# Kernel optimization log

Measured on AMD Instinct MI355X. Metric: run time of the kernel, lower is better.

The kernel has to match this reference:

```python
import jax, jax.numpy as jnp
import numpy as np

N_HEAD = 8


def setup_inputs() -> dict:
    key = jax.random.key(0)
    ks = jax.random.split(key, 12)
    b, l, d_q, d_o, h, w = 32, 64, 1024, 512, 32, 32

    def rn(k, shape, s=0.02):
        return jax.random.normal(k, shape, jnp.float32) * s

    return {
        "q": jax.random.normal(ks[0], (b, l, d_q), jnp.float32),
        "v": jax.random.normal(ks[1], (b, d_o, h, w), jnp.float32),
        "mask": jax.random.bernoulli(ks[2], 0.2, (b, l)),
        "w_qs_w": rn(ks[3], (d_o, d_q)), "w_qs_b": jnp.zeros((d_o,), jnp.float32),
        "w_qs_att_w": rn(ks[4], (1, d_o)), "w_qs_att_b": jnp.zeros((1,), jnp.float32),
        "w_kc_w": rn(ks[5], (d_o, d_o, 1, 1)), "w_kc_b": jnp.zeros((d_o,), jnp.float32),
        "w_kd_w": rn(ks[6], (d_o, d_o, 1, 1)), "w_kd_b": jnp.zeros((d_o,), jnp.float32),
        "w_vs_w": rn(ks[7], (d_o, d_o, 1, 1)), "w_vs_b": jnp.zeros((d_o,), jnp.float32),
        "w_m_w": rn(ks[8], (1, d_o, 3, 3)), "w_m_b": jnp.zeros((1,), jnp.float32),
        "bn_gamma": jnp.ones((d_o,), jnp.float32), "bn_beta": jnp.zeros((d_o,), jnp.float32),
        "bn_mean": jnp.zeros((d_o,), jnp.float32), "bn_var": jnp.ones((d_o,), jnp.float32),
    }


def _conv1x1(x, wgt, bias):  # x: (b,c,h,w), wgt: (o,c,1,1)
    return jnp.einsum('bchw,oc->bohw', x, wgt[:, :, 0, 0]) + bias[None, :, None, None]


def reference(q, v, mask, w_qs_w, w_qs_b, w_qs_att_w, w_qs_att_b,
              w_kc_w, w_kc_b, w_kd_w, w_kd_b, w_vs_w, w_vs_b,
              w_m_w, w_m_b, bn_gamma, bn_beta, bn_mean, bn_var):
    b, l, _ = q.shape
    _, c, h, w_ = v.shape
    n = N_HEAD
    dk = c // n
    temp = float(np.power(dk, 0.5))  # sqrt(d_o // n_head)
    residual = v

    qp = q @ w_qs_w.T + w_qs_b                       # (b,l,d_o)
    flap = qp @ w_qs_att_w.T + w_qs_att_b            # (b,l,1)
    flap = jnp.where(mask[:, :, None], -1e9, flap)
    flap = jax.nn.softmax(flap, axis=-1)             # softmax over size-1 dim -> all ones (faithful to torch)

    kc = _conv1x1(v, w_kc_w, w_kc_b).reshape(b, n, dk, h * w_).transpose(0, 1, 3, 2)  # (b,n,hw,dk)
    kd = _conv1x1(v, w_kd_w, w_kd_b).reshape(b, n, dk, h * w_).transpose(0, 1, 3, 2)
    vh = _conv1x1(v, w_vs_w, w_vs_b).reshape(b, n, dk, h * w_).transpose(0, 1, 3, 2)
    qh = qp.reshape(b, l, n, dk).transpose(0, 2, 1, 3)                                 # (b,n,l,dk)

    # Collect: bmm -> weight by flap -> reduce over l -> softmax over hw -> bmm with v
    attn_col = jnp.einsum('bnld,bnsd->bnls', qh, kc)                 # (b,n,l,hw)
    attn_col = (attn_col * flap[:, None, :, :]).sum(axis=2, keepdims=True) / temp  # (b,n,1,hw)
    attn_col = jax.nn.softmax(attn_col, axis=-1)
    attn = jnp.einsum('bnus,bnsd->bnud', attn_col, vh)               # (b,n,1,dk)

    # Diffuse: bmm -> weight by flap^T -> reduce over l -> sigmoid -> outer product
    attn_dif = jnp.einsum('bnsd,bnld->bnsl', kd, qh)                 # (b,n,hw,l)
    flap_t = flap.transpose(0, 2, 1)[:, None]                        # (b,1,1,l)
    attn_dif = jax.nn.sigmoid((attn_dif * flap_t).sum(-1, keepdims=True) / temp)  # (b,n,hw,1)
    output = attn_dif * attn                                         # (b,n,hw,dk)

    # Faithful to torch permute(0,1,4,3,2).view(b,-1,h,w) (requires h==w)
    out = output.reshape(b, n, h, w_, dk).transpose(0, 1, 4, 3, 2).reshape(b, c, h, w_)
    attn_map = out

    m = jax.lax.conv_general_dilated(out, w_m_w, (1, 1), 'SAME',
                                     dimension_numbers=('NCHW', 'OIHW', 'NCHW'))
    m_attn = (m + w_m_b[None, :, None, None]).reshape(b, h * w_)

    eps = 1e-5  # BatchNorm2d eval mode
    scale = bn_gamma / jnp.sqrt(bn_var + eps)
    out = (out - bn_mean[None, :, None, None]) * scale[None, :, None, None] + bn_beta[None, :, None, None]
    out = out + residual
    out = jnp.where(out >= 0, out, 0.1 * out)  # LeakyReLU(0.1)
    return (out, m_attn, attn_map)
```

## Files before the change

kernel.cpp:

```cpp
#include <hip/hip_runtime.h>


#define BB 32
#define LL 64
#define DQn 1024
#define CCn 512
#define NH 8
#define DKn 64
#define HWn 1024
#define NBLK 512
#define SLOTSTRIDE 16

typedef unsigned short u16;
typedef unsigned int u32;
typedef unsigned long long u64;

__device__ __forceinline__ float bfr(u16 u) {
    return __uint_as_float(((u32)u) << 16);
}
__device__ __forceinline__ u16 f2bf(float f) {
    u32 x = __float_as_uint(f);
    u32 r = (x + 0x7FFFu + ((x >> 16) & 1u)) >> 16;
    return (u16)r;
}

__device__ __forceinline__ void cst(float* p, float v) {
    __hip_atomic_store(p, v, __ATOMIC_RELAXED, __HIP_MEMORY_SCOPE_AGENT);
}
__device__ __forceinline__ u32 cldu(const u32* p) {
    return __hip_atomic_load(const_cast<u32*>(p), __ATOMIC_RELAXED,
                             __HIP_MEMORY_SCOPE_AGENT);
}
__device__ __forceinline__ void cstu(u32* p, u32 v) {
    __hip_atomic_store(p, v, __ATOMIC_RELAXED, __HIP_MEMORY_SCOPE_AGENT);
}

#define POOLB 78080

struct MArgs {
    const float *q, *v, *wqs, *bqs, *wkc, *bkc, *wkd, *bkd, *wvs, *bvs, *wm, *wmb,
                *gam, *bet, *mea, *var;
    float *qsp, *qs, *wq, *bq, *dsig, *sums, *attn, *A2g, *pvp;
    u32* bar;
    float *out0, *out1, *out2;
};

__device__ __forceinline__ void gbar(u32* bar, int i) {
    u32* slots = bar + 16;
    u32 epoch = (u32)(i + 1);
    __syncthreads();
    int t = threadIdx.x;
    if (blockIdx.x == (u32)(NBLK - 1)) {
        if (t < 64) {
            if (t == 0) cstu(&slots[(NBLK - 1) * SLOTSTRIDE], epoch);
            int base = t * (NBLK / 64);
            int it = 0;
            for (;;) {
                bool ok = true;
#pragma unroll
                for (int k = 0; k < NBLK / 64; ++k)
                    ok = ok && (cldu(&slots[(base + k) * SLOTSTRIDE]) == epoch);
                if (__all(ok)) break;
                __builtin_amdgcn_s_sleep(1);
                if (++it > (1 << 15)) break;
            }
            if (t == 0) cstu(&bar[8 + i], 1u);
        }
    } else if (t == 0) {
        cstu(&slots[blockIdx.x * SLOTSTRIDE], epoch);
        int it = 0;
        while (cldu(&bar[8 + i]) == 0u) {
            __builtin_amdgcn_s_sleep(2);
            if (++it > (1 << 18)) break;
        }
    }
    __syncthreads();
    __builtin_amdgcn_fence(__ATOMIC_ACQUIRE, "agent");
}

__global__ void kinit(u32* bar) {
    int t = threadIdx.x + blockIdx.x * blockDim.x;
    int total = 16 + NBLK * SLOTSTRIDE;
    for (int i = t; i < total; i += blockDim.x * gridDim.x)
        cstu(&bar[i], 0u);
}

#define PVACC(accv, eA, eB, vf) \
    accv[0] += eA.x * (vf); accv[1] += eA.y * (vf); accv[2] += eA.z * (vf); accv[3] += eA.w * (vf); \
    accv[4] += eB.x * (vf); accv[5] += eB.y * (vf); accv[6] += eB.z * (vf); accv[7] += eB.w * (vf);

__global__ void __launch_bounds__(256, 2) mega(MArgs A) {
    extern __shared__ char pool[];
    u32*   vtd = (u32*)pool;
    float* red = (float*)(pool + 65536);
    float* etb = (float*)(pool + 69888);
    float* ext = (float*)(pool + 71936);
    float* scr2  = red;
    float* pvl   = etb;
    float* scr7  = red;
    float* al7   = red + 320;
    float* sinvp = red + 384;
    float* dsl   = red;
    float* A2l   = red + 512;
    u16*   k8s   = (u16*)etb;
    float* al    = ext;
    float* bnA   = ext + 512;
    float* bnB   = ext + 1024;

    int t = threadIdx.x;
    int bid = blockIdx.x;
    int sc = bid & 15, b = bid >> 4;
    int s0 = sc * 64;

    if (bid < 128) {
        int b1 = bid >> 2;
        int dq = (bid & 3) * 256 + t;
        const float* qp = A.q + (size_t)b1 * LL * DQn + dq;
        float acc = 0.f;
#pragma unroll 8
        for (int l = 0; l < LL; ++l) acc += qp[l * DQn];
        cst(&A.qsp[b1 * DQn + dq], acc);
    }

    {
        int sp = t & 31, c2 = t >> 5;
        const float* vb = A.v + (((size_t)(b * CCn + c2 * 64)) << 10) + s0 + sp * 2;
#pragma unroll 8
        for (int cr = 0; cr < 64; ++cr) {
            int r = c2 * 64 + cr;
            float2 xv = *reinterpret_cast<const float2*>(vb + ((size_t)cr << 10));
            u32 w = (u32)f2bf(xv.x) | ((u32)f2bf(xv.y) << 16);
            vtd[r * 32 + (sp ^ (r & 31))] = w;
        }
    }
    gbar(A.bar, 0);

    {
        int dof = bid;
        int b2 = t & 31, ch = t >> 5;
        const float* wrow = A.wqs + (size_t)dof * DQn + ch * 128;
        const float* qrow = A.qsp + (size_t)b2 * DQn + ch * 128;
        float acc = 0.f;
#pragma unroll 8
        for (int i = 0; i < 128; i += 4) {
            float4 wv = *reinterpret_cast<const float4*>(wrow + i);
            float4 qv = *reinterpret_cast<const float4*>(qrow + i);
            acc += wv.x * qv.x + wv.y * qv.y + wv.z * qv.z + wv.w * qv.w;
        }
        scr2[t] = acc;
        __syncthreads();
        if (t < 32) {
            float a = 0.f;
#pragma unroll
            for (int c2 = 0; c2 < 8; ++c2) a += scr2[c2 * 32 + t];
            cst(&A.qs[t * CCn + dof], a + 64.f * A.bqs[dof]);
        }
    }
    gbar(A.bar, 1);

    {
        float2 p = *reinterpret_cast<const float2*>(&A.qs[b * CCn + t * 2]);
        etb[t * 2] = p.x; etb[t * 2 + 1] = p.y;
    }
    __syncthreads();

    if (sc == 0 && t < 16) {
        int wsel = t >> 3, n = t & 7;
        const float* bw = wsel ? A.bkd : A.bkc;
        float a2 = 0.f;
#pragma unroll 8
        for (int d = 0; d < DKn; ++d)
            a2 += etb[n * DKn + d] * bw[n * DKn + d];
        cst(&A.bq[wsel * 256 + b * 8 + n], a2);
    }

    {
        int cl = t & 31, n3 = t >> 5;
        int c = sc * 32 + cl;
#pragma unroll
        for (int wsel = 0; wsel < 2; ++wsel) {
            const float* w = wsel ? A.wkd : A.wkc;
            const float* qrow = etb + n3 * DKn;
            const float* wrow = w + (size_t)(n3 * DKn) * CCn + c;
            float acc = 0.f;
#pragma unroll 8
            for (int d = 0; d < DKn; ++d) acc += qrow[d] * wrow[(size_t)d * CCn];
            cst(&A.wq[((size_t)b * CCn + c) * 16 + wsel * 8 + n3], acc);
        }
    }
    for (int i = t; i < 64 * 17; i += 256) red[i] = 0.f;
    gbar(A.bar, 2);

    {
        float* wqL = etb;
        int s = t & 63, g2 = t >> 6;
        int sp = s >> 1, sh = (s & 1) << 4;
        float ak[16];
#pragma unroll
        for (int j = 0; j < 16; ++j) ak[j] = 0.f;
#pragma unroll 1
        for (int cc4 = 0; cc4 < 4; ++cc4) {
            __syncthreads();
            {
                const float* src = A.wq + (((size_t)b * CCn + cc4 * 128) << 4) + t * 8;
                float4 p0 = *reinterpret_cast<const float4*>(src);
                float4 p1 = *reinterpret_cast<const float4*>(src + 4);
                float* dst = wqL + t * 8;
                dst[0] = p0.x; dst[1] = p0.y; dst[2] = p0.z; dst[3] = p0.w;
                dst[4] = p1.x; dst[5] = p1.y; dst[6] = p1.z; dst[7] = p1.w;
            }
            __syncthreads();
#pragma unroll 4
            for (int i = 0; i < 32; ++i) {
                int cl = g2 * 32 + i;
                int r = cc4 * 128 + cl;
                u32 wv = vtd[r * 32 + (sp ^ (r & 31))];
                float vvf = bfr((u16)(wv >> sh));
                const float* wc = wqL + cl * 16;
#pragma unroll
                for (int j = 0; j < 16; ++j) ak[j] += wc[j] * vvf;
            }
        }
#pragma unroll
        for (int j = 0; j < 16; ++j) atomicAdd(&red[s * 17 + j], ak[j]);
    }
    __syncthreads();
    if (t < 64) {
        int s = t;
#pragma unroll
        for (int n = 0; n < NH; ++n) {
            float rc = red[s * 17 + n];
            float rd = red[s * 17 + 8 + n];
            float skc = (rc + A.bq[b * 8 + n]) * 0.125f;
            float skd = (rd + A.bq[256 + b * 8 + n]) * 0.125f;
            etb[s * 8 + n] = __expf(skc);
            cst(&A.dsig[((size_t)(b * NH + n)) * HWn + s0 + s],
                1.f / (1.f + __expf(-skd)));
        }
    }
    __syncthreads();
    if (t < 8) {
        float a = 0.f;
#pragma unroll
        for (int s = 0; s < 64; ++s) a += etb[s * 8 + t];
        cst(&A.sums[(b * NH + t) * 16 + sc], a);
    }
    {
        float acc0[NH], acc1[NH];
#pragma unroll
        for (int n = 0; n < NH; ++n) { acc0[n] = 0.f; acc1[n] = 0.f; }
        int c0 = t, c1 = t + 256;
        int m = t & 31;
#pragma unroll 2
        for (int sp = 0; sp < 32; ++sp) {
            u32 w0 = vtd[c0 * 32 + (sp ^ m)];
            u32 w1 = vtd[c1 * 32 + (sp ^ m)];
            float va0 = bfr((u16)(w0 & 0xffffu)), va1 = bfr((u16)(w0 >> 16));
            float vb0 = bfr((u16)(w1 & 0xffffu)), vb1 = bfr((u16)(w1 >> 16));
            float4 e0a = *reinterpret_cast<const float4*>(etb + sp * 16);
            float4 e0b = *reinterpret_cast<const float4*>(etb + sp * 16 + 4);
            float4 e1a = *reinterpret_cast<const float4*>(etb + sp * 16 + 8);
            float4 e1b = *reinterpret_cast<const float4*>(etb + sp * 16 + 12);
            PVACC(acc0, e0a, e0b, va0)
            PVACC(acc0, e1a, e1b, va1)
            PVACC(acc1, e0a, e0b, vb0)
            PVACC(acc1, e1a, e1b, vb1)
        }
        size_t base = ((size_t)sc * BB + b) * NH;
#pragma unroll
        for (int n = 0; n < NH; ++n) {
            cst(&A.pvp[(base + n) * CCn + c0], acc0[n]);
            cst(&A.pvp[(base + n) * CCn + c1], acc1[n]);
        }
    }
    gbar(A.bar, 3);

    if (bid < 256) {
        int n = bid & 7, b7 = bid >> 3;
        for (int c = t; c < CCn; c += 256) {
            float acc = 0.f;
#pragma unroll 4
            for (int s2 = 0; s2 < 16; ++s2)
                acc += A.pvp[(((size_t)s2 * BB + b7) * NH + n) * CCn + c];
            pvl[c] = acc;
        }
        if (t == 0) {
            float a = 0.f;
#pragma unroll
            for (int s2 = 0; s2 < 16; ++s2)
                a += A.sums[(b7 * NH + n) * 16 + s2];
            sinvp[0] = 1.f / a;
        }
        __syncthreads();
        {
            int d = t & 63, qq = t >> 6;
            const float* wrow = A.wvs + (size_t)(n * DKn + d) * CCn + qq * 128;
            const float* pq = pvl + qq * 128;
            float acc = 0.f;
#pragma unroll 4
            for (int i = 0; i < 128; ++i) acc += pq[i] * wrow[i];
            scr7[d * 5 + qq] = acc;
        }
        __syncthreads();
        if (t < 64) {
            float a = (scr7[t * 5] + scr7[t * 5 + 1] + scr7[t * 5 + 2] + scr7[t * 5 + 3])
                      * sinvp[0] + A.bvs[n * DKn + t];
            cst(&A.attn[(b7 * NH + n) * DKn + t], a);
            al7[t] = a;
        }
        __syncthreads();
        if (t < 9) {
            float acc = 0.f;
#pragma unroll 8
            for (int d2 = 0; d2 < DKn; ++d2)
                acc += al7[d2] * A.wm[(n * DKn + d2) * 9 + t];
            cst(&A.A2g[b7 * 72 + n * 9 + t], acc);
        }
    }
    gbar(A.bar, 4);

    int y0 = sc * 2;
    {
        for (int idx = t; idx < CCn; idx += 256) {
            al[idx] = A.attn[b * CCn + idx];
            float Av = A.gam[idx] * rsqrtf(A.var[idx] + 1e-5f);
            bnA[idx] = Av;
            bnB[idx] = A.bet[idx] - A.mea[idx] * Av;
        }
        for (int idx = t; idx < NH * 64; idx += 256) {
            int n = idx >> 6, r6 = idx & 63;
            int yb2 = r6 >> 5, x = r6 & 31;
            dsl[idx] = A.dsig[((size_t)(b * NH + n)) * HWn + x * 32 + y0 + yb2];
        }
        for (int idx = t; idx < 4 * NH * 32; idx += 256) {
            int ry = idx >> 8, n = (idx >> 5) & 7, x = idx & 31;
            int ycol = y0 - 1 + ry;
            float dvv = 0.f;
            if ((unsigned)ycol < 32u)
                dvv = A.dsig[((size_t)(b * NH + n)) * HWn + x * 32 + ycol];
            k8s[idx] = f2bf(dvv);
        }
        if (t < 72) A2l[t] = A.A2g[b * 72 + t];
    }
    __syncthreads();
    {
        int l = t & 63, wv = t >> 6;
        int csub = l >> 4, yb = (l >> 3) & 1, x0 = (l & 7) * 4;
        int sl = yb * 32 + x0;
#pragma unroll 2
        for (int it = 0; it < 32; ++it) {
            int c = it * 16 + wv * 4 + csub;
            int n = c >> 6;
            int m = c & 31;
            u32 w0 = vtd[c * 32 + ((sl >> 1) ^ m)];
            u32 w1 = vtd[c * 32 + (((sl >> 1) + 1) ^ m)];
            float4 dv = *reinterpret_cast<const float4*>(dsl + n * 64 + sl);
            float a = al[c], Ac = bnA[c], Bc = bnB[c];
            float p0 = a * dv.x, p1 = a * dv.y, p2 = a * dv.z, p3 = a * dv.w;
            size_t ob = (((size_t)(b * CCn + c)) << 10) + (u32)((y0 + yb) * 32 + x0);
            *reinterpret_cast<float4*>(A.out2 + ob) = make_float4(p0, p1, p2, p3);
            float o0 = fmaf(p0, Ac, Bc) + bfr((u16)(w0 & 0xffffu));
            float o1 = fmaf(p1, Ac, Bc) + bfr((u16)(w0 >> 16));
            float o2 = fmaf(p2, Ac, Bc) + bfr((u16)(w1 & 0xffffu));
            float o3 = fmaf(p3, Ac, Bc) + bfr((u16)(w1 >> 16));
            o0 = o0 < 0.f ? 0.1f * o0 : o0;
            o1 = o1 < 0.f ? 0.1f * o1 : o1;
            o2 = o2 < 0.f ? 0.1f * o2 : o2;
            o3 = o3 < 0.f ? 0.1f * o3 : o3;
            *reinterpret_cast<float4*>(A.out0 + ob) = make_float4(o0, o1, o2, o3);
        }
    }
    if (t < 64) {
        int y = y0 + (t >> 5), x = t & 31;
        float msum = 0.f;
#pragma unroll
        for (int n = 0; n < NH; ++n) {
#pragma unroll
            for (int dy = 0; dy < 3; ++dy) {
                int ry = (t >> 5) + dy;
#pragma unroll
                for (int dx = 0; dx < 3; ++dx) {
                    int xx = x + dx - 1;
                    if ((unsigned)xx < 32u)
                        msum += A2l[n * 9 + dy * 3 + dx] * bfr(k8s[ry * 256 + n * 32 + xx]);
                }
            }
        }
        A.out1[b * HWn + y * 32 + x] = msum + A.wmb[0];
    }
}


__global__ void k1_qsum_pre(const float* __restrict__ q, float* __restrict__ qsp) {
    int b = blockIdx.y;
    int dq = blockIdx.x * 256 + threadIdx.x;
    const float* qp = q + (size_t)b * LL * DQn + dq;
    float acc = 0.f;
#pragma unroll 8
    for (int l = 0; l < LL; ++l) acc += qp[l * DQn];
    qsp[b * DQn + dq] = acc;
}

__global__ void k2_qsum(const float* __restrict__ qsp, const float* __restrict__ w,
                        const float* __restrict__ bias, float* __restrict__ qs) {
    int dof = blockIdx.x;
    int t = threadIdx.x;
    int b = t & 31, ch = t >> 5;
    const float* wrow = w + (size_t)dof * DQn + ch * 128;
    const float* qrow = qsp + (size_t)b * DQn + ch * 128;
    float acc = 0.f;
#pragma unroll 8
    for (int i = 0; i < 128; i += 4) {
        float4 wv = *reinterpret_cast<const float4*>(wrow + i);
        float4 qv = *reinterpret_cast<const float4*>(qrow + i);
        acc += wv.x * qv.x + wv.y * qv.y + wv.z * qv.z + wv.w * qv.w;
    }
    __shared__ float scr[256];
    scr[t] = acc;
    __syncthreads();
    if (t < 32) {
        float a = 0.f;
#pragma unroll
        for (int c2 = 0; c2 < 8; ++c2) a += scr[c2 * 32 + t];
        qs[t * CCn + dof] = a + 64.f * bias[dof];
    }
}

__global__ void k3_wq(const float* __restrict__ qs,
                      const float* __restrict__ wkc, const float* __restrict__ bkc,
                      const float* __restrict__ wkd, const float* __restrict__ bkd,
                      float* __restrict__ wq, float* __restrict__ bq) {
    int cc = blockIdx.x, wsel = blockIdx.y, b = blockIdx.z;
    const float* w = wsel ? wkd : wkc;
    int cl = threadIdx.x & 31, n = threadIdx.x >> 5;
    int c = cc * 32 + cl;
    const float* qrow = qs + b * CCn + n * DKn;
    const float* wrow = w + (size_t)(n * DKn) * CCn + c;
    float acc = 0.f;
#pragma unroll 8
    for (int d = 0; d < DKn; ++d)
        acc += qrow[d] * wrow[(size_t)d * CCn];
    wq[((size_t)b * CCn + c) * 16 + wsel * 8 + n] = acc;
    if (cc == 0 && b == 0) {
        const float* bw = wsel ? bkd : bkc;
        int pp = threadIdx.x, bb = pp >> 3, nn = pp & 7;
        float a2 = 0.f;
#pragma unroll 8
        for (int d = 0; d < DKn; ++d)
            a2 += qs[bb * CCn + nn * DKn + d] * bw[nn * DKn + d];
        bq[wsel * 256 + pp] = a2;
    }
}

__global__ void __launch_bounds__(256) k46_scorepv(
        const float* __restrict__ v, const float* __restrict__ wq,
        const float* __restrict__ bq, float* __restrict__ dsig,
        float* __restrict__ pvp, float* __restrict__ sums) {
    int sc = blockIdx.x, b = blockIdx.y;
    __shared__ u16 vt[CCn * 33];
    __shared__ float red[4][32][17];
    __shared__ float et[32 * 8];
    int t = threadIdx.x;
    int s0 = sc * 32;
    {
        int s = t & 31, c2 = t >> 5;
        const float* vb = v + ((size_t)(b * CCn + c2 * 64) << 10) + s0 + s;
#pragma unroll 8
        for (int cr = 0; cr < 64; ++cr)
            vt[(c2 * 64 + cr) * 33 + s] = f2bf(vb[(size_t)cr << 10]);
    }
    __syncthreads();
    {
        int s = t & 31, g = t >> 5;
        float ak[16];
#pragma unroll
        for (int j = 0; j < 16; ++j) ak[j] = 0.f;
        const float* wqb = wq + ((size_t)b * CCn + g * 64) * 16;
#pragma unroll 4
        for (int i = 0; i < 64; ++i) {
            float vv = bfr(vt[(g * 64 + i) * 33 + s]);
            const float* wc = wqb + i * 16;
#pragma unroll
            for (int j = 0; j < 16; ++j) ak[j] += wc[j] * vv;
        }
#pragma unroll
        for (int j = 0; j < 16; ++j) ak[j] += __shfl_xor(ak[j], 32);
        int wv = t >> 6;
        if ((t & 63) < 32) {
#pragma unroll
            for (int j = 0; j < 16; ++j) red[wv][s][j] = ak[j];
        }
    }
    __syncthreads();
    if (t < 32) {
        int s = t;
#pragma unroll
        for (int n = 0; n < NH; ++n) {
            float rc = red[0][s][n] + red[1][s][n] + red[2][s][n] + red[3][s][n];
            float rd = red[0][s][8 + n] + red[1][s][8 + n] + red[2][s][8 + n] + red[3][s][8 + n];
            float skc = (rc + bq[b * 8 + n]) * 0.125f;
            float skd = (rd + bq[256 + b * 8 + n]) * 0.125f;
            et[s * 8 + n] = __expf(skc);
            dsig[(b * NH + n) * HWn + s0 + s] = 1.f / (1.f + __expf(-skd));
        }
    }
    __syncthreads();
    if (t < 8) {
        float a = 0.f;
#pragma unroll
        for (int s = 0; s < 32; ++s) a += et[s * 8 + t];
        sums[(b * NH + t) * 32 + sc] = a;
    }
    {
        float acc0[NH], acc1[NH];
#pragma unroll
        for (int n = 0; n < NH; ++n) { acc0[n] = 0.f; acc1[n] = 0.f; }
#pragma unroll 2
        for (int s = 0; s < 32; ++s) {
            float4 ea = *reinterpret_cast<const float4*>(et + s * 8);
            float4 eb = *reinterpret_cast<const float4*>(et + s * 8 + 4);
            float va = bfr(vt[t * 33 + s]);
            float vb2 = bfr(vt[(t + 256) * 33 + s]);
            acc0[0] += ea.x * va; acc0[1] += ea.y * va; acc0[2] += ea.z * va; acc0[3] += ea.w * va;
            acc0[4] += eb.x * va; acc0[5] += eb.y * va; acc0[6] += eb.z * va; acc0[7] += eb.w * va;
            acc1[0] += ea.x * vb2; acc1[1] += ea.y * vb2; acc1[2] += ea.z * vb2; acc1[3] += ea.w * vb2;
            acc1[4] += eb.x * vb2; acc1[5] += eb.y * vb2; acc1[6] += eb.z * vb2; acc1[7] += eb.w * vb2;
        }
        size_t base = ((size_t)sc * BB + b) * NH;
#pragma unroll
        for (int n = 0; n < NH; ++n) {
            pvp[(base + n) * CCn + t] = acc0[n];
            pvp[(base + n) * CCn + t + 256] = acc1[n];
        }
    }
}

__global__ void k7_attn(const float* __restrict__ pvp, const float* __restrict__ sums,
                        const float* __restrict__ wvs, const float* __restrict__ bvs,
                        float* __restrict__ attn) {
    int n = blockIdx.x, b = blockIdx.y;
    __shared__ float pvl[CCn];
    __shared__ float scr[64 * 5];
    __shared__ float sinv;
    int t = threadIdx.x;
    if (t == 0) {
        float a = 0.f;
#pragma unroll
        for (int sc = 0; sc < 32; ++sc) a += sums[(b * NH + n) * 32 + sc];
        sinv = 1.f / a;
    }
    for (int c = t; c < CCn; c += 256) {
        float acc = 0.f;
#pragma unroll 4
        for (int sc = 0; sc < 32; ++sc)
            acc += pvp[(((size_t)sc * BB + b) * NH + n) * CCn + c];
        pvl[c] = acc;
    }
    __syncthreads();
    int d = t & 63, qq = t >> 6;
    const float* wrow = wvs + (size_t)(n * DKn + d) * CCn + qq * 128;
    const float* pq = pvl + qq * 128;
    float acc = 0.f;
#pragma unroll 4
    for (int i = 0; i < 128; ++i) acc += pq[i] * wrow[i];
    scr[d * 5 + qq] = acc;
    __syncthreads();
    if (t < 64) {
        float a = (scr[t * 5] + scr[t * 5 + 1] + scr[t * 5 + 2] + scr[t * 5 + 3]) * sinv
                + bvs[n * DKn + t];
        attn[(b * NH + n) * DKn + t] = a;
    }
}

__global__ void k8_mattn(const float* __restrict__ dsig, const float* __restrict__ attn,
                         const float* __restrict__ wm, const float* __restrict__ wmb,
                         float* __restrict__ out1) {
    int b = blockIdx.x;
    __shared__ float dst[NH * 1056];
    __shared__ float al[CCn];
    __shared__ float A2[NH * 9];
    int t = threadIdx.x;
    al[t] = attn[b * CCn + t];
    al[t + 256] = attn[b * CCn + t + 256];
    for (int g = t; g < NH * HWn; g += 256) {
        int n = g >> 10, s = g & 1023;
        dst[n * 1056 + (s & 31) * 33 + (s >> 5)] = dsig[b * NH * HWn + g];
    }
    __syncthreads();
    if (t < 72) {
        int n = t / 9, tap = t % 9;
        float acc = 0.f;
#pragma unroll 8
        for (int d = 0; d < DKn; ++d)
            acc += al[n * DKn + d] * wm[(n * DKn + d) * 9 + tap];
        A2[t] = acc;
    }
    __syncthreads();
    float bm = wmb[0];
    for (int pos = t; pos < HWn; pos += 256) {
        int y = pos >> 5, x = pos & 31;
        float m = 0.f;
#pragma unroll
        for (int n = 0; n < NH; ++n) {
            const float* dn = dst + n * 1056;
#pragma unroll
            for (int dy = 0; dy < 3; ++dy) {
                int yy = y + dy - 1;
                if ((unsigned)yy < 32u) {
#pragma unroll
                    for (int dx = 0; dx < 3; ++dx) {
                        int xx = x + dx - 1;
                        if ((unsigned)xx < 32u)
                            m += A2[n * 9 + dy * 3 + dx] * dn[yy * 33 + xx];
                    }
                }
            }
        }
        out1[b * HWn + pos] = m + bm;
    }
}

__global__ void __launch_bounds__(256) k9_out(
        const float* __restrict__ v, const float* __restrict__ dsig,
        const float* __restrict__ attn,
        const float* __restrict__ gamma, const float* __restrict__ beta,
        const float* __restrict__ mean, const float* __restrict__ var,
        float* __restrict__ out0, float* __restrict__ out2) {
    int dh = blockIdx.x, n = blockIdx.y, b = blockIdx.z;
    __shared__ float dst[1056];
    __shared__ float al[16], bnA[16], bnB[16];
    int t = threadIdx.x;
#pragma unroll
    for (int k = 0; k < 4; ++k) {
        int s = t + k * 256;
        dst[(s & 31) * 33 + (s >> 5)] = dsig[(b * NH + n) * HWn + s];
    }
    if (t < 16) {
        int d = dh * 16 + t;
        al[t] = attn[(b * NH + n) * DKn + d];
        int ch = n * DKn + d;
        float A = gamma[ch] * rsqrtf(var[ch] + 1e-5f);
        bnA[t] = A;
        bnB[t] = beta[ch] - mean[ch] * A;
    }
    __syncthreads();
    int y = t >> 3, x = (t & 7) * 4;
    const float* dr = dst + y * 33 + x;
#pragma unroll 2
    for (int k = 0; k < 16; ++k) {
        int d = dh * 16 + k;
        size_t base = (((size_t)(b * CCn + n * DKn + d)) << 10) + y * 32 + x;
        float4 v4 = *reinterpret_cast<const float4*>(v + base);
        float a = al[k], A = bnA[k], Bc = bnB[k];
        float p0 = a * dr[0], p1 = a * dr[1], p2 = a * dr[2], p3 = a * dr[3];
        float4 mo = make_float4(p0, p1, p2, p3);
        *reinterpret_cast<float4*>(out2 + base) = mo;
        float o0 = p0 * A + Bc + v4.x;
        float o1 = p1 * A + Bc + v4.y;
        float o2 = p2 * A + Bc + v4.z;
        float o3 = p3 * A + Bc + v4.w;
        o0 = o0 < 0.f ? 0.1f * o0 : o0;
        o1 = o1 < 0.f ? 0.1f * o1 : o1;
        o2 = o2 < 0.f ? 0.1f * o2 : o2;
        o3 = o3 < 0.f ? 0.1f * o3 : o3;
        float4 oo = make_float4(o0, o1, o2, o3);
        *reinterpret_cast<float4*>(out0 + base) = oo;
    }
}

extern "C" void kernel_launch(void* const* d_in, const int* in_sizes, int n_in,
                              void* d_out, int out_size, void* d_ws, size_t ws_size,
                              hipStream_t stream) {
    (void)in_sizes; (void)n_in; (void)out_size; (void)ws_size;
    const float* q   = (const float*)d_in[0];
    const float* v   = (const float*)d_in[1];
    const float* wqs = (const float*)d_in[3];
    const float* bqs = (const float*)d_in[4];
    const float* wkc = (const float*)d_in[7];
    const float* bkc = (const float*)d_in[8];
    const float* wkd = (const float*)d_in[9];
    const float* bkd = (const float*)d_in[10];
    const float* wvs = (const float*)d_in[11];
    const float* bvs = (const float*)d_in[12];
    const float* wm  = (const float*)d_in[13];
    const float* wmb = (const float*)d_in[14];
    const float* gam = (const float*)d_in[15];
    const float* bet = (const float*)d_in[16];
    const float* mea = (const float*)d_in[17];
    const float* var = (const float*)d_in[18];

    float* ws = (float*)d_ws;
    float* out0 = (float*)d_out;
    float* out1 = out0 + 16777216;
    float* out2 = out1 + 32768;

    static int mode = -1;
    if (mode < 0) {
        hipError_t e = hipFuncSetAttribute(reinterpret_cast<const void*>(mega),
                                           hipFuncAttributeMaxDynamicSharedMemorySize,
                                           POOLB);
        mode = (e == hipSuccess) ? 1 : 0;
    }

    if (mode == 1) {
        MArgs a;
        a.q = q; a.v = v; a.wqs = wqs; a.bqs = bqs; a.wkc = wkc; a.bkc = bkc;
        a.wkd = wkd; a.bkd = bkd; a.wvs = wvs; a.bvs = bvs; a.wm = wm; a.wmb = wmb;
        a.gam = gam; a.bet = bet; a.mea = mea; a.var = var;
        a.qsp  = ws;
        a.qs   = ws + 32768;
        a.wq   = ws + 49152;
        a.bq   = ws + 311296;
        a.dsig = ws + 311808;
        a.sums = ws + 573952;
        a.attn = ws + 578048;
        a.A2g  = ws + 594432;
        a.pvp  = ws + 596736;
        a.bar  = (u32*)(ws + 2693888);
        a.out0 = out0; a.out1 = out1; a.out2 = out2;
        kinit<<<dim3(8), dim3(256), 0, stream>>>(a.bar);
        mega<<<dim3(NBLK), dim3(256), POOLB, stream>>>(a);
        return;
    }

    float* qsp  = ws + 0;
    float* qs   = ws + 32768;
    float* wq   = ws + 49152;
    float* bq   = ws + 311296;
    float* dsig = ws + 311808;
    float* sums = ws + 573952;
    float* attn = ws + 582144;
    float* pvp  = ws + 598528;

    k1_qsum_pre<<<dim3(4, 32), 256, 0, stream>>>(q, qsp);
    k2_qsum<<<dim3(512), 256, 0, stream>>>(qsp, wqs, bqs, qs);
    k3_wq<<<dim3(16, 2, 32), 256, 0, stream>>>(qs, wkc, bkc, wkd, bkd, wq, bq);
    k46_scorepv<<<dim3(32, 32), 256, 0, stream>>>(v, wq, bq, dsig, pvp, sums);
    k7_attn<<<dim3(8, 32), 256, 0, stream>>>(pvp, sums, wvs, bvs, attn);
    k8_mattn<<<dim3(32), 256, 0, stream>>>(dsig, attn, wm, wmb, out1);
    k9_out<<<dim3(4, 8, 32), 256, 0, stream>>>(v, dsig, attn, gam, bet, mea, var, out0, out2);
}
```

Before: 401.6 us.

## Replace grid-wide barriers with per-batch 16-block group barriers

```diff
diff --git a/kernel.cpp b/kernel.cpp
--- a/kernel.cpp
+++ b/kernel.cpp
@@ -45,42 +45,28 @@
     float *out0, *out1, *out2;
 };
 
-__device__ __forceinline__ void gbar(u32* bar, int i) {
-    u32* slots = bar + 16;
+__device__ __forceinline__ void gbarb(u32* slots, int b, int sc, int i) {
     u32 epoch = (u32)(i + 1);
     __syncthreads();
     int t = threadIdx.x;
-    if (blockIdx.x == (u32)(NBLK - 1)) {
-        if (t < 64) {
-            if (t == 0) cstu(&slots[(NBLK - 1) * SLOTSTRIDE], epoch);
-            int base = t * (NBLK / 64);
-            int it = 0;
-            for (;;) {
-                bool ok = true;
-#pragma unroll
-                for (int k = 0; k < NBLK / 64; ++k)
-                    ok = ok && (cldu(&slots[(base + k) * SLOTSTRIDE]) == epoch);
-                if (__all(ok)) break;
-                __builtin_amdgcn_s_sleep(1);
-                if (++it > (1 << 15)) break;
-            }
-            if (t == 0) cstu(&bar[8 + i], 1u);
-        }
-    } else if (t == 0) {
-        cstu(&slots[blockIdx.x * SLOTSTRIDE], epoch);
+    if (t < 64) {
+        if (t == 0) cstu(&slots[(b * 16 + sc) * SLOTSTRIDE], epoch);
         int it = 0;
-        while (cldu(&bar[8 + i]) == 0u) {
-            __builtin_amdgcn_s_sleep(2);
-            if (++it > (1 << 18)) break;
-        }
-    }
-    __syncthreads();
-    __builtin_amdgcn_fence(__ATOMIC_ACQUIRE, "agent");
+        for (;;) {
+            bool ok = true;
+            if (t < 16)
+                ok = (cldu(&slots[(b * 16 + t) * SLOTSTRIDE]) >= epoch);
+            if (__all(ok)) break;
+            __builtin_amdgcn_s_sleep(1);
+            if (++it > (1 << 17)) break;
+        }
+    }
+    __syncthreads();
 }
 
 __global__ void kinit(u32* bar) {
     int t = threadIdx.x + blockIdx.x * blockDim.x;
-    int total = 16 + NBLK * SLOTSTRIDE;
+    int total = NBLK * SLOTSTRIDE;
     for (int i = t; i < total; i += blockDim.x * gridDim.x)
         cstu(&bar[i], 0u);
 }
@@ -90,12 +76,12 @@
     accv[4] += eB.x * (vf); accv[5] += eB.y * (vf); accv[6] += eB.z * (vf); accv[7] += eB.w * (vf);
 
 __global__ void __launch_bounds__(256, 2) mega(MArgs A) {
+    __builtin_amdgcn_fence(__ATOMIC_ACQUIRE, "agent");
     extern __shared__ char pool[];
     u32*   vtd = (u32*)pool;
     float* red = (float*)(pool + 65536);
     float* etb = (float*)(pool + 69888);
     float* ext = (float*)(pool + 71936);
-    float* scr2  = red;
     float* pvl   = etb;
     float* scr7  = red;
     float* al7   = red + 320;
@@ -111,15 +97,21 @@
     int bid = blockIdx.x;
     int sc = bid & 15, b = bid >> 4;
     int s0 = sc * 64;
-
-    if (bid < 128) {
-        int b1 = bid >> 2;
-        int dq = (bid & 3) * 256 + t;
-        const float* qp = A.q + (size_t)b1 * LL * DQn + dq;
+    u32* slots = A.bar;
+
+    {
+        int dqo = t & 63, lq = t >> 6;
+        const float* qp = A.q + (size_t)b * (LL * DQn) + (size_t)(lq * 16) * DQn
+                        + sc * 64 + dqo;
         float acc = 0.f;
-#pragma unroll 8
-        for (int l = 0; l < LL; ++l) acc += qp[l * DQn];
-        cst(&A.qsp[b1 * DQn + dq], acc);
+#pragma unroll
+        for (int l = 0; l < 16; ++l) acc += qp[(size_t)l * DQn];
+        red[dqo * 4 + lq] = acc;
+    }
+    __syncthreads();
+    if (t < 64) {
+        float a = red[t * 4] + red[t * 4 + 1] + red[t * 4 + 2] + red[t * 4 + 3];
+        cst(&A.qsp[b * DQn + sc * 64 + t], a);
     }
 
     {
@@ -133,30 +125,26 @@
             vtd[r * 32 + (sp ^ (r & 31))] = w;
         }
     }
-    gbar(A.bar, 0);
-
-    {
-        int dof = bid;
-        int b2 = t & 31, ch = t >> 5;
-        const float* wrow = A.wqs + (size_t)dof * DQn + ch * 128;
-        const float* qrow = A.qsp + (size_t)b2 * DQn + ch * 128;
+    gbarb(slots, b, sc, 0);
+
+    {
+        int dof = sc * 32 + (t >> 3);
+        int part = t & 7;
+        const float* qrow = A.qsp + b * DQn + part * 128;
+        const float* wrow = A.wqs + (size_t)dof * DQn + part * 128;
         float acc = 0.f;
 #pragma unroll 8
         for (int i = 0; i < 128; i += 4) {
+            float4 qv = *reinterpret_cast<const float4*>(qrow + i);
             float4 wv = *reinterpret_cast<const float4*>(wrow + i);
-            float4 qv = *reinterpret_cast<const float4*>(qrow + i);
             acc += wv.x * qv.x + wv.y * qv.y + wv.z * qv.z + wv.w * qv.w;
         }
-        scr2[t] = acc;
-        __syncthreads();
-        if (t < 32) {
-            float a = 0.f;
-#pragma unroll
-            for (int c2 = 0; c2 < 8; ++c2) a += scr2[c2 * 32 + t];
-            cst(&A.qs[t * CCn + dof], a + 64.f * A.bqs[dof]);
-        }
-    }
-    gbar(A.bar, 1);
+        acc += __shfl_xor(acc, 4);
+        acc += __shfl_xor(acc, 2);
+        acc += __shfl_xor(acc, 1);
+        if (part == 0) cst(&A.qs[b * CCn + dof], acc + 64.f * A.bqs[dof]);
+    }
+    gbarb(slots, b, sc, 1);
 
     {
         float2 p = *reinterpret_cast<const float2*>(&A.qs[b * CCn + t * 2]);
@@ -171,7 +159,7 @@
 #pragma unroll 8
         for (int d = 0; d < DKn; ++d)
             a2 += etb[n * DKn + d] * bw[n * DKn + d];
-        cst(&A.bq[wsel * 256 + b * 8 + n], a2);
+        cst(&A.bq[b * 32 + wsel * 8 + n], a2);
     }
 
     {
@@ -189,7 +177,7 @@
         }
     }
     for (int i = t; i < 64 * 17; i += 256) red[i] = 0.f;
-    gbar(A.bar, 2);
+    gbarb(slots, b, sc, 2);
 
     {
         float* wqL = etb;
@@ -231,8 +219,8 @@
         for (int n = 0; n < NH; ++n) {
             float rc = red[s * 17 + n];
             float rd = red[s * 17 + 8 + n];
-            float skc = (rc + A.bq[b * 8 + n]) * 0.125f;
-            float skd = (rd + A.bq[256 + b * 8 + n]) * 0.125f;
+            float skc = (rc + A.bq[b * 32 + n]) * 0.125f;
+            float skd = (rd + A.bq[b * 32 + 8 + n]) * 0.125f;
             etb[s * 8 + n] = __expf(skc);
             cst(&A.dsig[((size_t)(b * NH + n)) * HWn + s0 + s],
                 1.f / (1.f + __expf(-skd)));
@@ -273,22 +261,22 @@
             cst(&A.pvp[(base + n) * CCn + c1], acc1[n]);
         }
     }
-    gbar(A.bar, 3);
-
-    if (bid < 256) {
-        int n = bid & 7, b7 = bid >> 3;
+    gbarb(slots, b, sc, 3);
+
+    if (sc < 8) {
+        int n = sc;
         for (int c = t; c < CCn; c += 256) {
             float acc = 0.f;
 #pragma unroll 4
             for (int s2 = 0; s2 < 16; ++s2)
-                acc += A.pvp[(((size_t)s2 * BB + b7) * NH + n) * CCn + c];
+                acc += A.pvp[(((size_t)s2 * BB + b) * NH + n) * CCn + c];
             pvl[c] = acc;
         }
         if (t == 0) {
             float a = 0.f;
 #pragma unroll
             for (int s2 = 0; s2 < 16; ++s2)
-                a += A.sums[(b7 * NH + n) * 16 + s2];
+                a += A.sums[(b * NH + n) * 16 + s2];
             sinvp[0] = 1.f / a;
         }
         __syncthreads();
@@ -305,7 +293,7 @@
         if (t < 64) {
             float a = (scr7[t * 5] + scr7[t * 5 + 1] + scr7[t * 5 + 2] + scr7[t * 5 + 3])
                       * sinvp[0] + A.bvs[n * DKn + t];
-            cst(&A.attn[(b7 * NH + n) * DKn + t], a);
+            cst(&A.attn[(b * NH + n) * DKn + t], a);
             al7[t] = a;
         }
         __syncthreads();
@@ -314,10 +302,10 @@
 #pragma unroll 8
             for (int d2 = 0; d2 < DKn; ++d2)
                 acc += al7[d2] * A.wm[(n * DKn + d2) * 9 + t];
-            cst(&A.A2g[b7 * 72 + n * 9 + t], acc);
-        }
-    }
-    gbar(A.bar, 4);
+            cst(&A.A2g[b * 96 + n * 9 + t], acc);
+        }
+    }
+    gbarb(slots, b, sc, 4);
 
     int y0 = sc * 2;
     {
@@ -340,7 +328,7 @@
                 dvv = A.dsig[((size_t)(b * NH + n)) * HWn + x * 32 + ycol];
             k8s[idx] = f2bf(dvv);
         }
-        if (t < 72) A2l[t] = A.A2g[b * 72 + t];
+        if (t < 72) A2l[t] = A.A2g[b * 96 + t];
     }
     __syncthreads();
     {
@@ -711,12 +699,12 @@
         a.qs   = ws + 32768;
         a.wq   = ws + 49152;
         a.bq   = ws + 311296;
-        a.dsig = ws + 311808;
-        a.sums = ws + 573952;
-        a.attn = ws + 578048;
-        a.A2g  = ws + 594432;
-        a.pvp  = ws + 596736;
-        a.bar  = (u32*)(ws + 2693888);
+        a.dsig = ws + 312320;
+        a.sums = ws + 574464;
+        a.attn = ws + 578560;
+        a.A2g  = ws + 594944;
+        a.pvp  = ws + 598016;
+        a.bar  = (u32*)(ws + 2695168);
         a.out0 = out0; a.out1 = out1; a.out2 = out2;
         kinit<<<dim3(8), dim3(256), 0, stream>>>(a.bar);
         mega<<<dim3(NBLK), dim3(256), POOLB, stream>>>(a);
```

After: 323.6 us. 1.24x faster.
